# Optimization experiments

Measured on AMD Instinct MI355X. Metric: run time of the kernel, lower is better.

The kernel has to match this reference:

```python
import jax, jax.numpy as jnp
import numpy as np
from jax import lax

V, H, A, S = 256, 2048, 512, 512  # vocab, hidden, attn, seq_len


def setup_inputs() -> dict:
    key = jax.random.key(0)
    ks = jax.random.split(key, 8)
    sc = 0.02  # small init to keep tanh unsaturated
    return {
        "x_enc": jax.random.normal(ks[0], (S, V), jnp.float32),
        "x_dec": jax.random.normal(ks[1], (S, V), jnp.float32),
        "W_enc": jax.random.normal(ks[2], (H, V + H), jnp.float32) * sc,
        "b_enc": jnp.zeros((H,), jnp.float32),
        "Wa_enc": jax.random.normal(ks[3], (A, H), jnp.float32) * sc,
        "Wa_dec": jax.random.normal(ks[4], (A, H), jnp.float32) * sc,
        "v_a": jax.random.normal(ks[5], (A,), jnp.float32) * sc,
        "W_dec": jax.random.normal(ks[6], (H, V + 2 * H), jnp.float32) * sc,
        "b_dec": jnp.zeros((H,), jnp.float32),
        "W_out": jax.random.normal(ks[7], (V, H), jnp.float32) * sc,
        "b_out": jnp.zeros((V,), jnp.float32),
    }


def reference(x_enc, x_dec, W_enc, b_enc, Wa_enc, Wa_dec, v_a, W_dec, b_dec, W_out, b_out):
    h0 = jnp.zeros((W_enc.shape[0],), x_enc.dtype)

    # Encoder: h_t = tanh(W_enc [x_t ; h_{t-1}] + b)
    def enc_step(h, x):
        h_new = jnp.tanh(jnp.concatenate([x, h]) @ W_enc.T + b_enc)
        return h_new, h_new

    h_enc, enc_states = lax.scan(enc_step, h0, x_enc)  # enc_states: (S, H)

    # Encoder-side attention projection is step-invariant -> hoist (same math).
    enc_proj = enc_states @ Wa_enc.T  # (S, A)

    # Decoder with per-step Bahdanau additive attention.
    def dec_step(h, x):
        dec_proj = h @ Wa_dec.T                              # (A,)
        energy = jnp.tanh(enc_proj + dec_proj) @ v_a         # (S,)
        attn_w = jax.nn.softmax(energy)                      # (S,)
        context = attn_w @ enc_states                        # (H,)
        h_new = jnp.tanh(jnp.concatenate([x, context, h]) @ W_dec.T + b_dec)
        logits = h_new @ W_out.T + b_out                     # (V,)
        return h_new, logits

    _, outputs = lax.scan(dec_step, h_enc, x_dec)  # (S, V)
    return outputs
```

## Files before the change

kernel.cpp:

```cpp
#include <hip/hip_runtime.h>

#define V 256
#define H 2048
#define A 512
#define S 512
#define NBLK 128
#define NTHR 512

typedef float f32x4 __attribute__((ext_vector_type(4)));
typedef float f32x2 __attribute__((ext_vector_type(2)));

__device__ __forceinline__ f32x4 ldg_cg4(const float* p) {
    f32x4 r;
    asm volatile("global_load_dwordx4 %0, %1, off sc0 sc1\n\ts_waitcnt vmcnt(0)"
                 : "=v"(r) : "v"(p) : "memory");
    return r;
}
__device__ __forceinline__ void stg_cg1(float* p, float v) {
    asm volatile("global_store_dword %0, %1, off sc0 sc1" :: "v"(p), "v"(v) : "memory");
}
__device__ __forceinline__ void stg_cg2(float* p, f32x2 v) {
    asm volatile("global_store_dwordx2 %0, %1, off sc0 sc1" :: "v"(p), "v"(v) : "memory");
}

__device__ __forceinline__ void gbar(int* base, int e) {
    __syncthreads();
    if (threadIdx.x == 0) {
        asm volatile("s_waitcnt vmcnt(0)" ::: "memory");
        int* leaf = base + ((blockIdx.x & 7) << 6);
        int prev = __hip_atomic_fetch_add(leaf, 1, __ATOMIC_RELAXED, __HIP_MEMORY_SCOPE_AGENT);
        if (prev == e * (NBLK / 8) - 1) {
            int p2 = __hip_atomic_fetch_add(base + 512, 1, __ATOMIC_RELAXED, __HIP_MEMORY_SCOPE_AGENT);
            if (p2 == e * 8 - 1)
                __hip_atomic_store(base + 576, e, __ATOMIC_RELAXED, __HIP_MEMORY_SCOPE_AGENT);
        }
        while (__hip_atomic_load(base + 576, __ATOMIC_RELAXED, __HIP_MEMORY_SCOPE_AGENT) < e)
            __builtin_amdgcn_s_sleep(1);
    }
    __syncthreads();
}

__global__ void init_bar(int* bar) {
    for (int i = threadIdx.x; i < 2048; i += blockDim.x) bar[i] = 0;
}

__global__ __launch_bounds__(256) void gemm_nt(
    const float* __restrict__ Amat, int lda,
    const float* __restrict__ Bmat, int ldb,
    float* __restrict__ C, int ldc,
    const float* __restrict__ bias, int M, int N, int K)
{
    __shared__ float As[16][68];
    __shared__ float Bs[16][68];
    const int tid = threadIdx.x;
    const int tx = tid & 15;
    const int ty = tid >> 4;
    const int m0 = blockIdx.y * 64;
    const int n0 = blockIdx.x * 64;
    const int lr = tid >> 2;
    const int lk = (tid & 3) * 4;

    float acc[4][4] = {};
    for (int k0 = 0; k0 < K; k0 += 16) {
        float4 av = *(const float4*)(Amat + (size_t)(m0 + lr) * lda + k0 + lk);
        float4 bv = *(const float4*)(Bmat + (size_t)(n0 + lr) * ldb + k0 + lk);
        __syncthreads();
        As[lk+0][lr] = av.x; As[lk+1][lr] = av.y; As[lk+2][lr] = av.z; As[lk+3][lr] = av.w;
        Bs[lk+0][lr] = bv.x; Bs[lk+1][lr] = bv.y; Bs[lk+2][lr] = bv.z; Bs[lk+3][lr] = bv.w;
        __syncthreads();
        #pragma unroll
        for (int k = 0; k < 16; ++k) {
            float a4[4], b4[4];
            #pragma unroll
            for (int i = 0; i < 4; ++i) a4[i] = As[k][ty*4+i];
            #pragma unroll
            for (int j = 0; j < 4; ++j) b4[j] = Bs[k][tx*4+j];
            #pragma unroll
            for (int i = 0; i < 4; ++i)
                #pragma unroll
                for (int j = 0; j < 4; ++j) acc[i][j] += a4[i] * b4[j];
        }
    }
    #pragma unroll
    for (int i = 0; i < 4; ++i) {
        const int m = m0 + ty*4 + i;
        #pragma unroll
        for (int j = 0; j < 4; ++j) {
            const int n = n0 + tx*4 + j;
            float v = acc[i][j];
            if (bias) v += bias[n];
            C[(size_t)m * ldc + n] = v;
        }
    }
}

__global__ __launch_bounds__(NTHR, 2) void enc_scan(
    const float* __restrict__ W_enc, const float* __restrict__ accx,
    float* __restrict__ states, int* bar)
{
    __shared__ __align__(16) float hs[H];
    const int tid = threadIdx.x;
    const int wid = tid >> 6, lane = tid & 63;
    const int w   = blockIdx.x * 8 + wid;
    const int r0  = 2*w, r1 = 2*w + 1;
    int epoch = 0;

    f32x4 we0[8], we1[8];
    #pragma unroll
    for (int k = 0; k < 8; ++k) {
        we0[k] = *(const f32x4*)(W_enc + (size_t)r0*(V+H) + V + 4*(lane + 64*k));
        we1[k] = *(const f32x4*)(W_enc + (size_t)r1*(V+H) + V + 4*(lane + 64*k));
    }
    const f32x4* hs4 = (const f32x4*)hs;

    if (lane == 0) {
        f32x2 h0; h0.x = tanhf(accx[r0]); h0.y = tanhf(accx[r1]);
        stg_cg2(states + 2*w, h0);
    }

    for (int t = 1; t < S; ++t) {
        gbar(bar, ++epoch);
        ((f32x4*)hs)[tid] = ldg_cg4(states + (size_t)(t-1)*H + 4*tid);
        __syncthreads();
        float a0 = 0.f, a1 = 0.f;
        #pragma unroll
        for (int k = 0; k < 8; ++k) {
            f32x4 hv = hs4[lane + 64*k];
            a0 += we0[k].x*hv.x + we0[k].y*hv.y + we0[k].z*hv.z + we0[k].w*hv.w;
            a1 += we1[k].x*hv.x + we1[k].y*hv.y + we1[k].z*hv.z + we1[k].w*hv.w;
        }
        #pragma unroll
        for (int off = 32; off; off >>= 1) { a0 += __shfl_down(a0, off); a1 += __shfl_down(a1, off); }
        if (lane == 0) {
            f32x2 hv;
            hv.x = tanhf(a0 + accx[(size_t)t*H + r0]);
            hv.y = tanhf(a1 + accx[(size_t)t*H + r1]);
            stg_cg2(states + (size_t)t*H + 2*w, hv);
        }
    }
}

__global__ __launch_bounds__(NTHR, 2) void dec_scan(
    const float* __restrict__ Wa_dec, const float* __restrict__ W_dec,
    const float* __restrict__ enc_proj, const float* __restrict__ v_a,
    const float* __restrict__ WcT, const float* __restrict__ accx,
    const float* __restrict__ enc_states, float* __restrict__ h_dec,
    float* __restrict__ dec_proj, float* __restrict__ evec,
    int* bar)
{
    __shared__ __align__(16) float hs[H];
    __shared__ __align__(16) float ps[A];
    __shared__ __align__(16) float es[S];
    __shared__ float zred[8];
    const int tid = threadIdx.x;
    const int wid = tid >> 6, lane = tid & 63;
    const int w   = blockIdx.x * 8 + wid;
    const int r0  = 2*w, r1 = 2*w + 1;
    int epoch = 0;

    f32x4 wh0[8], wh1[8], wa[8], wc0[2], wc1[2], ep[2], va[2];
    #pragma unroll
    for (int k = 0; k < 8; ++k) {
        wh0[k] = *(const f32x4*)(W_dec + (size_t)r0*(V+2*H) + V + H + 4*(lane + 64*k));
        wh1[k] = *(const f32x4*)(W_dec + (size_t)r1*(V+2*H) + V + H + 4*(lane + 64*k));
        wa[k]  = (f32x4)(0.f);
    }
    #pragma unroll
    for (int k = 0; k < 2; ++k) {
        wc0[k] = *(const f32x4*)(WcT + (size_t)r0*S + 4*(lane + 64*k));
        wc1[k] = *(const f32x4*)(WcT + (size_t)r1*S + 4*(lane + 64*k));
        ep[k] = (f32x4)(0.f); va[k] = (f32x4)(0.f);
    }
    if (w < A) {
        #pragma unroll
        for (int k = 0; k < 8; ++k)
            wa[k] = *(const f32x4*)(Wa_dec + (size_t)w*H + 4*(lane + 64*k));
        #pragma unroll
        for (int k = 0; k < 2; ++k) {
            ep[k] = *(const f32x4*)(enc_proj + (size_t)w*A + 4*(lane + 64*k));
            va[k] = *(const f32x4*)(v_a + 4*(lane + 64*k));
        }
    }
    const f32x4* hs4 = (const f32x4*)hs;
    const f32x4* ps4 = (const f32x4*)ps;
    const f32x4* es4 = (const f32x4*)es;

    for (int t = 0; t < S; ++t) {
        const float* hsrc = t ? (h_dec + (size_t)(t-1)*H) : (enc_states + (size_t)(S-1)*H);
        ((f32x4*)hs)[tid] = ldg_cg4(hsrc + 4*tid);
        __syncthreads();

        float aH0 = 0.f, aH1 = 0.f, aP = 0.f;
        #pragma unroll
        for (int k = 0; k < 8; ++k) {
            f32x4 hv = hs4[lane + 64*k];
            aH0 += wh0[k].x*hv.x + wh0[k].y*hv.y + wh0[k].z*hv.z + wh0[k].w*hv.w;
            aH1 += wh1[k].x*hv.x + wh1[k].y*hv.y + wh1[k].z*hv.z + wh1[k].w*hv.w;
            aP  += wa[k].x*hv.x  + wa[k].y*hv.y  + wa[k].z*hv.z  + wa[k].w*hv.w;
        }
        #pragma unroll
        for (int off = 32; off; off >>= 1) {
            aH0 += __shfl_down(aH0, off);
            aH1 += __shfl_down(aH1, off);
            aP  += __shfl_down(aP,  off);
        }
        if (w < A && lane == 0) stg_cg1(dec_proj + w, aP);
        gbar(bar, ++epoch);

        if (tid < A/4) ((f32x4*)ps)[tid] = ldg_cg4(dec_proj + 4*tid);
        __syncthreads();
        if (w < S) {
            float e_ = 0.f;
            #pragma unroll
            for (int k = 0; k < 2; ++k) {
                f32x4 p = ps4[lane + 64*k];
                e_ += va[k].x*tanhf(ep[k].x + p.x) + va[k].y*tanhf(ep[k].y + p.y)
                    + va[k].z*tanhf(ep[k].z + p.z) + va[k].w*tanhf(ep[k].w + p.w);
            }
            #pragma unroll
            for (int off = 32; off; off >>= 1) e_ += __shfl_down(e_, off);
            if (lane == 0) stg_cg1(evec + w, expf(e_));
        }
        gbar(bar, ++epoch);

        if (tid < S/4) ((f32x4*)es)[tid] = ldg_cg4(evec + 4*tid);
        __syncthreads();
        float z = es[tid];
        #pragma unroll
        for (int off = 32; off; off >>= 1) z += __shfl_down(z, off);
        if (lane == 0) zred[wid] = z;
        __syncthreads();
        const float Z = zred[0]+zred[1]+zred[2]+zred[3]+zred[4]+zred[5]+zred[6]+zred[7];
        float c0 = 0.f, c1 = 0.f;
        #pragma unroll
        for (int k = 0; k < 2; ++k) {
            f32x4 ev = es4[lane + 64*k];
            c0 += wc0[k].x*ev.x + wc0[k].y*ev.y + wc0[k].z*ev.z + wc0[k].w*ev.w;
            c1 += wc1[k].x*ev.x + wc1[k].y*ev.y + wc1[k].z*ev.z + wc1[k].w*ev.w;
        }
        #pragma unroll
        for (int off = 32; off; off >>= 1) { c0 += __shfl_down(c0, off); c1 += __shfl_down(c1, off); }
        if (lane == 0) {
            const float Zi = 1.f / Z;
            f32x2 hv;
            hv.x = tanhf(accx[(size_t)t*H + r0] + aH0 + c0*Zi);
            hv.y = tanhf(accx[(size_t)t*H + r1] + aH1 + c1*Zi);
            stg_cg2(h_dec + (size_t)t*H + 2*w, hv);
        }
        if (t < S-1) gbar(bar, ++epoch);
    }
}

extern "C" void kernel_launch(void* const* d_in, const int* in_sizes, int n_in,
                              void* d_out, int out_size, void* d_ws, size_t ws_size,
                              hipStream_t stream) {
    const float* x_enc  = (const float*)d_in[0];
    const float* x_dec  = (const float*)d_in[1];
    const float* W_enc  = (const float*)d_in[2];
    const float* b_enc  = (const float*)d_in[3];
    const float* Wa_enc = (const float*)d_in[4];
    const float* Wa_dec = (const float*)d_in[5];
    const float* v_a    = (const float*)d_in[6];
    const float* W_dec  = (const float*)d_in[7];
    const float* b_dec  = (const float*)d_in[8];
    const float* W_out  = (const float*)d_in[9];
    const float* b_out  = (const float*)d_in[10];
    float* out = (float*)d_out;

    float* ws         = (float*)d_ws;
    float* accx_enc   = ws;
    float* enc_states = accx_enc + (size_t)S*H;
    float* enc_proj   = enc_states + (size_t)S*H;
    float* WcT        = enc_proj + (size_t)S*A;
    float* accx_dec   = WcT + (size_t)H*S;
    float* h_dec      = accx_dec + (size_t)S*H;
    float* dec_proj   = h_dec + (size_t)S*H;
    float* evec       = dec_proj + A;
    int*   bar        = (int*)(evec + S);
    int* bar_e = bar;
    int* bar_d = bar + 1024;

    dim3 b256(256);

    init_bar<<<1, 256, 0, stream>>>(bar);

    gemm_nt<<<dim3(H/64, S/64), b256, 0, stream>>>(x_enc, V, W_enc, V+H, accx_enc, H, b_enc, S, H, V);
    gemm_nt<<<dim3(H/64, S/64), b256, 0, stream>>>(x_dec, V, W_dec, V+2*H, accx_dec, H, b_dec, S, H, V);

    {
        const float* We = W_enc; const float* ax = accx_enc; float* st = enc_states; int* bb = bar_e;
        void* args[] = { &We, &ax, &st, &bb };
        hipLaunchCooperativeKernel((void*)enc_scan, dim3(NBLK), dim3(NTHR), args, 0, stream);
    }

    gemm_nt<<<dim3(A/64, S/64), b256, 0, stream>>>(enc_states, H, Wa_enc, H, enc_proj, A, nullptr, S, A, H);
    gemm_nt<<<dim3(S/64, H/64), b256, 0, stream>>>(W_dec + V, V+2*H, enc_states, H, WcT, S, nullptr, H, S, H);

    {
        const float* wa = Wa_dec; const float* wd = W_dec; const float* epj = enc_proj;
        const float* vv = v_a; const float* wc = WcT; const float* ax = accx_dec;
        const float* est = enc_states; float* hd = h_dec; float* dp = dec_proj; float* ev = evec;
        int* bb = bar_d;
        void* args[] = { &wa, &wd, &epj, &vv, &wc, &ax, &est, &hd, &dp, &ev, &bb };
        hipLaunchCooperativeKernel((void*)dec_scan, dim3(NBLK), dim3(NTHR), args, 0, stream);
    }

    gemm_nt<<<dim3(V/64, S/64), b256, 0, stream>>>(h_dec, H, W_out, H, out, V, b_out, S, V, H);
}
```

Before: 6.806 ms.

## Replace grid barriers with tagged-data flag polling in encoder and decoder scans

Removes the hierarchical atomic grid barrier. Each producer now writes its values together with a step tag into double-buffered exchange slots, and consumers spin until every chunk they need carries the current tag. This turns each global barrier into point-to-point data-ready waits and lets blocks that finished early proceed. The attention-projection and energy work is moved onto the first 64 blocks so the others skip it. The cost is more global load traffic from polling and heavier read contention on the exchange buffers.

```diff
diff --git a/kernel.cpp b/kernel.cpp
--- a/kernel.cpp
+++ b/kernel.cpp
@@ -8,40 +8,33 @@
 #define NTHR 512
 
 typedef float f32x4 __attribute__((ext_vector_type(4)));
-typedef float f32x2 __attribute__((ext_vector_type(2)));
-
-__device__ __forceinline__ f32x4 ldg_cg4(const float* p) {
+
+__device__ __forceinline__ void st_chunk(float* p, float x, float y, int tag) {
+    f32x4 v; v.x = x; v.y = y; v.z = 0.f; v.w = __int_as_float(tag);
+    asm volatile("global_store_dwordx4 %0, %1, off sc0 sc1" :: "v"(p), "v"(v) : "memory");
+}
+__device__ __forceinline__ f32x4 poll1(const float* p, int tag) {
     f32x4 r;
-    asm volatile("global_load_dwordx4 %0, %1, off sc0 sc1\n\ts_waitcnt vmcnt(0)"
-                 : "=v"(r) : "v"(p) : "memory");
-    return r;
-}
-__device__ __forceinline__ void stg_cg1(float* p, float v) {
-    asm volatile("global_store_dword %0, %1, off sc0 sc1" :: "v"(p), "v"(v) : "memory");
-}
-__device__ __forceinline__ void stg_cg2(float* p, f32x2 v) {
-    asm volatile("global_store_dwordx2 %0, %1, off sc0 sc1" :: "v"(p), "v"(v) : "memory");
-}
-
-__device__ __forceinline__ void gbar(int* base, int e) {
-    __syncthreads();
-    if (threadIdx.x == 0) {
-        asm volatile("s_waitcnt vmcnt(0)" ::: "memory");
-        int* leaf = base + ((blockIdx.x & 7) << 6);
-        int prev = __hip_atomic_fetch_add(leaf, 1, __ATOMIC_RELAXED, __HIP_MEMORY_SCOPE_AGENT);
-        if (prev == e * (NBLK / 8) - 1) {
-            int p2 = __hip_atomic_fetch_add(base + 512, 1, __ATOMIC_RELAXED, __HIP_MEMORY_SCOPE_AGENT);
-            if (p2 == e * 8 - 1)
-                __hip_atomic_store(base + 576, e, __ATOMIC_RELAXED, __HIP_MEMORY_SCOPE_AGENT);
-        }
-        while (__hip_atomic_load(base + 576, __ATOMIC_RELAXED, __HIP_MEMORY_SCOPE_AGENT) < e)
-            __builtin_amdgcn_s_sleep(1);
-    }
-    __syncthreads();
-}
-
-__global__ void init_bar(int* bar) {
-    for (int i = threadIdx.x; i < 2048; i += blockDim.x) bar[i] = 0;
+    for (;;) {
+        asm volatile("global_load_dwordx4 %0, %1, off sc0 sc1\n\ts_waitcnt vmcnt(0)"
+                     : "=v"(r) : "v"(p) : "memory");
+        if (__float_as_int(r.w) == tag) return r;
+    }
+}
+__device__ __forceinline__ void poll2(const float* p0, const float* p1, int tag,
+                                      f32x4& a, f32x4& b) {
+    for (;;) {
+        asm volatile("global_load_dwordx4 %0, %2, off sc0 sc1\n\t"
+                     "global_load_dwordx4 %1, %3, off sc0 sc1\n\t"
+                     "s_waitcnt vmcnt(0)"
+                     : "=v"(a), "=v"(b) : "v"(p0), "v"(p1) : "memory");
+        if (__float_as_int(a.w) == tag && __float_as_int(b.w) == tag) return;
+    }
+}
+
+__global__ void init_ex(float* p, int n) {
+    int i = blockIdx.x * blockDim.x + threadIdx.x;
+    if (i < n) p[i] = 0.f;
 }
 
 __global__ __launch_bounds__(256) void gemm_nt(
@@ -96,14 +89,13 @@
 
 __global__ __launch_bounds__(NTHR, 2) void enc_scan(
     const float* __restrict__ W_enc, const float* __restrict__ accx,
-    float* __restrict__ states, int* bar)
+    float* __restrict__ states, float* __restrict__ hex)
 {
-    __shared__ __align__(16) float hs[H];
+    __shared__ __align__(16) float hs[2][H];
     const int tid = threadIdx.x;
     const int wid = tid >> 6, lane = tid & 63;
     const int w   = blockIdx.x * 8 + wid;
-    const int r0  = 2*w, r1 = 2*w + 1;
-    int epoch = 0;
+    const int r0  = 2*w, r1 = r0 + 1;
 
     f32x4 we0[8], we1[8];
     #pragma unroll
@@ -111,31 +103,37 @@
         we0[k] = *(const f32x4*)(W_enc + (size_t)r0*(V+H) + V + 4*(lane + 64*k));
         we1[k] = *(const f32x4*)(W_enc + (size_t)r1*(V+H) + V + 4*(lane + 64*k));
     }
-    const f32x4* hs4 = (const f32x4*)hs;
 
     if (lane == 0) {
-        f32x2 h0; h0.x = tanhf(accx[r0]); h0.y = tanhf(accx[r1]);
-        stg_cg2(states + 2*w, h0);
+        float h0 = tanhf(accx[r0]), h1 = tanhf(accx[r1]);
+        states[r0] = h0; states[r1] = h1;
+        st_chunk(hex + 4*w, h0, h1, 1);
     }
 
     for (int t = 1; t < S; ++t) {
-        gbar(bar, ++epoch);
-        ((f32x4*)hs)[tid] = ldg_cg4(states + (size_t)(t-1)*H + 4*tid);
-        __syncthreads();
+        f32x4 ca, cb;
+        const float* hb = hex + ((t-1)&1)*4096;
+        poll2(hb + 8*tid, hb + 8*tid + 4, t, ca, cb);
+        float* dst = hs[t&1];
+        dst[4*tid+0] = ca.x; dst[4*tid+1] = ca.y;
+        dst[4*tid+2] = cb.x; dst[4*tid+3] = cb.y;
+        __syncthreads();
+
+        const f32x4* h4 = (const f32x4*)hs[t&1];
         float a0 = 0.f, a1 = 0.f;
         #pragma unroll
         for (int k = 0; k < 8; ++k) {
-            f32x4 hv = hs4[lane + 64*k];
+            f32x4 hv = h4[lane + 64*k];
             a0 += we0[k].x*hv.x + we0[k].y*hv.y + we0[k].z*hv.z + we0[k].w*hv.w;
             a1 += we1[k].x*hv.x + we1[k].y*hv.y + we1[k].z*hv.z + we1[k].w*hv.w;
         }
         #pragma unroll
         for (int off = 32; off; off >>= 1) { a0 += __shfl_down(a0, off); a1 += __shfl_down(a1, off); }
         if (lane == 0) {
-            f32x2 hv;
-            hv.x = tanhf(a0 + accx[(size_t)t*H + r0]);
-            hv.y = tanhf(a1 + accx[(size_t)t*H + r1]);
-            stg_cg2(states + (size_t)t*H + 2*w, hv);
+            float h0 = tanhf(a0 + accx[(size_t)t*H + r0]);
+            float h1 = tanhf(a1 + accx[(size_t)t*H + r1]);
+            states[(size_t)t*H + r0] = h0; states[(size_t)t*H + r1] = h1;
+            st_chunk(hex + (t&1)*4096 + 4*w, h0, h1, t+1);
         }
     }
 }
@@ -145,8 +143,7 @@
     const float* __restrict__ enc_proj, const float* __restrict__ v_a,
     const float* __restrict__ WcT, const float* __restrict__ accx,
     const float* __restrict__ enc_states, float* __restrict__ h_dec,
-    float* __restrict__ dec_proj, float* __restrict__ evec,
-    int* bar)
+    float* __restrict__ hexd, float* __restrict__ dpex, float* __restrict__ eex)
 {
     __shared__ __align__(16) float hs[H];
     __shared__ __align__(16) float ps[A];
@@ -155,8 +152,8 @@
     const int tid = threadIdx.x;
     const int wid = tid >> 6, lane = tid & 63;
     const int w   = blockIdx.x * 8 + wid;
-    const int r0  = 2*w, r1 = 2*w + 1;
-    int epoch = 0;
+    const int r0  = 2*w, r1 = r0 + 1;
+    const bool attn_blk = (blockIdx.x < 64);
 
     f32x4 wh0[8], wh1[8], wa[8], wc0[2], wc1[2], ep[2], va[2];
     #pragma unroll
@@ -171,7 +168,7 @@
         wc1[k] = *(const f32x4*)(WcT + (size_t)r1*S + 4*(lane + 64*k));
         ep[k] = (f32x4)(0.f); va[k] = (f32x4)(0.f);
     }
-    if (w < A) {
+    if (attn_blk) {
         #pragma unroll
         for (int k = 0; k < 8; ++k)
             wa[k] = *(const f32x4*)(Wa_dec + (size_t)w*H + 4*(lane + 64*k));
@@ -186,30 +183,42 @@
     const f32x4* es4 = (const f32x4*)es;
 
     for (int t = 0; t < S; ++t) {
-        const float* hsrc = t ? (h_dec + (size_t)(t-1)*H) : (enc_states + (size_t)(S-1)*H);
-        ((f32x4*)hs)[tid] = ldg_cg4(hsrc + 4*tid);
-        __syncthreads();
-
-        float aH0 = 0.f, aH1 = 0.f, aP = 0.f;
+        if (t == 0) {
+            ((f32x4*)hs)[tid] = ((const f32x4*)(enc_states + (size_t)(S-1)*H))[tid];
+        } else {
+            f32x4 ca, cb;
+            const float* hb = hexd + ((t-1)&1)*4096;
+            poll2(hb + 8*tid, hb + 8*tid + 4, t, ca, cb);
+            hs[4*tid+0] = ca.x; hs[4*tid+1] = ca.y;
+            hs[4*tid+2] = cb.x; hs[4*tid+3] = cb.y;
+        }
+        __syncthreads();
+
+        if (attn_blk) {
+            float aP = 0.f;
+            #pragma unroll
+            for (int k = 0; k < 8; ++k) {
+                f32x4 hv = hs4[lane + 64*k];
+                aP += wa[k].x*hv.x + wa[k].y*hv.y + wa[k].z*hv.z + wa[k].w*hv.w;
+            }
+            #pragma unroll
+            for (int off = 32; off; off >>= 1) aP += __shfl_down(aP, off);
+            if (lane == 0) st_chunk(dpex + (t&1)*2048 + 4*w, aP, 0.f, t+1);
+        }
+        float aH0 = 0.f, aH1 = 0.f;
         #pragma unroll
         for (int k = 0; k < 8; ++k) {
             f32x4 hv = hs4[lane + 64*k];
             aH0 += wh0[k].x*hv.x + wh0[k].y*hv.y + wh0[k].z*hv.z + wh0[k].w*hv.w;
             aH1 += wh1[k].x*hv.x + wh1[k].y*hv.y + wh1[k].z*hv.z + wh1[k].w*hv.w;
-            aP  += wa[k].x*hv.x  + wa[k].y*hv.y  + wa[k].z*hv.z  + wa[k].w*hv.w;
-        }
-        #pragma unroll
-        for (int off = 32; off; off >>= 1) {
-            aH0 += __shfl_down(aH0, off);
-            aH1 += __shfl_down(aH1, off);
-            aP  += __shfl_down(aP,  off);
-        }
-        if (w < A && lane == 0) stg_cg1(dec_proj + w, aP);
-        gbar(bar, ++epoch);
-
-        if (tid < A/4) ((f32x4*)ps)[tid] = ldg_cg4(dec_proj + 4*tid);
-        __syncthreads();
-        if (w < S) {
+        }
+        #pragma unroll
+        for (int off = 32; off; off >>= 1) { aH0 += __shfl_down(aH0, off); aH1 += __shfl_down(aH1, off); }
+
+        if (attn_blk) {
+            f32x4 c = poll1(dpex + (t&1)*2048 + 4*tid, t+1);
+            ps[tid] = c.x;
+            __syncthreads();
             float e_ = 0.f;
             #pragma unroll
             for (int k = 0; k < 2; ++k) {
@@ -219,18 +228,22 @@
             }
             #pragma unroll
             for (int off = 32; off; off >>= 1) e_ += __shfl_down(e_, off);
-            if (lane == 0) stg_cg1(evec + w, expf(e_));
-        }
-        gbar(bar, ++epoch);
-
-        if (tid < S/4) ((f32x4*)es)[tid] = ldg_cg4(evec + 4*tid);
-        __syncthreads();
+            if (lane == 0) st_chunk(eex + (t&1)*2048 + 4*w, expf(e_), 0.f, t+1);
+        }
+
+        {
+            f32x4 c = poll1(eex + (t&1)*2048 + 4*tid, t+1);
+            es[tid] = c.x;
+        }
+        __syncthreads();
+
         float z = es[tid];
         #pragma unroll
         for (int off = 32; off; off >>= 1) z += __shfl_down(z, off);
         if (lane == 0) zred[wid] = z;
         __syncthreads();
         const float Z = zred[0]+zred[1]+zred[2]+zred[3]+zred[4]+zred[5]+zred[6]+zred[7];
+
         float c0 = 0.f, c1 = 0.f;
         #pragma unroll
         for (int k = 0; k < 2; ++k) {
@@ -242,12 +255,11 @@
         for (int off = 32; off; off >>= 1) { c0 += __shfl_down(c0, off); c1 += __shfl_down(c1, off); }
         if (lane == 0) {
             const float Zi = 1.f / Z;
-            f32x2 hv;
-            hv.x = tanhf(accx[(size_t)t*H + r0] + aH0 + c0*Zi);
-            hv.y = tanhf(accx[(size_t)t*H + r1] + aH1 + c1*Zi);
-            stg_cg2(h_dec + (size_t)t*H + 2*w, hv);
-        }
-        if (t < S-1) gbar(bar, ++epoch);
+            float h0 = tanhf(accx[(size_t)t*H + r0] + aH0 + c0*Zi);
+            float h1 = tanhf(accx[(size_t)t*H + r1] + aH1 + c1*Zi);
+            h_dec[(size_t)t*H + r0] = h0; h_dec[(size_t)t*H + r1] = h1;
+            st_chunk(hexd + (t&1)*4096 + 4*w, h0, h1, t+1);
+        }
     }
 }
 
@@ -274,22 +286,22 @@
     float* WcT        = enc_proj + (size_t)S*A;
     float* accx_dec   = WcT + (size_t)H*S;
     float* h_dec      = accx_dec + (size_t)S*H;
-    float* dec_proj   = h_dec + (size_t)S*H;
-    float* evec       = dec_proj + A;
-    int*   bar        = (int*)(evec + S);
-    int* bar_e = bar;
-    int* bar_d = bar + 1024;
+    float* hex_e      = h_dec + (size_t)S*H;
+    float* hex_d      = hex_e + 8192;
+    float* dp_ex      = hex_d + 8192;
+    float* e_ex       = dp_ex + 4096;
+    const int n_ex = 8192 + 8192 + 4096 + 4096;
 
     dim3 b256(256);
 
-    init_bar<<<1, 256, 0, stream>>>(bar);
+    init_ex<<<dim3((n_ex + 255)/256), b256, 0, stream>>>(hex_e, n_ex);
 
     gemm_nt<<<dim3(H/64, S/64), b256, 0, stream>>>(x_enc, V, W_enc, V+H, accx_enc, H, b_enc, S, H, V);
     gemm_nt<<<dim3(H/64, S/64), b256, 0, stream>>>(x_dec, V, W_dec, V+2*H, accx_dec, H, b_dec, S, H, V);
 
     {
-        const float* We = W_enc; const float* ax = accx_enc; float* st = enc_states; int* bb = bar_e;
-        void* args[] = { &We, &ax, &st, &bb };
+        const float* We = W_enc; const float* ax = accx_enc; float* st = enc_states; float* hx = hex_e;
+        void* args[] = { &We, &ax, &st, &hx };
         hipLaunchCooperativeKernel((void*)enc_scan, dim3(NBLK), dim3(NTHR), args, 0, stream);
     }
 
@@ -299,9 +311,9 @@
     {
         const float* wa = Wa_dec; const float* wd = W_dec; const float* epj = enc_proj;
         const float* vv = v_a; const float* wc = WcT; const float* ax = accx_dec;
-        const float* est = enc_states; float* hd = h_dec; float* dp = dec_proj; float* ev = evec;
-        int* bb = bar_d;
-        void* args[] = { &wa, &wd, &epj, &vv, &wc, &ax, &est, &hd, &dp, &ev, &bb };
+        const float* est = enc_states; float* hd = h_dec;
+        float* hx = hex_d; float* dx = dp_ex; float* ex = e_ex;
+        void* args[] = { &wa, &wd, &epj, &vv, &wc, &ax, &est, &hd, &hx, &dx, &ex };
         hipLaunchCooperativeKernel((void*)dec_scan, dim3(NBLK), dim3(NTHR), args, 0, stream);
     }
 
```

Measured after the change: 7.142 ms. 1.05x slower.
